# Kernel optimization log

Measured on AMD Instinct MI355X. Metric: run time of the kernel, lower is better.

Reference implementation:

```python
import jax, jax.numpy as jnp
import numpy as np

NUM_CHUNKS = 8
IGNORE_INDEX = -100


def setup_inputs() -> dict:
    key = jax.random.key(0)
    k1, k2, k3, k4 = jax.random.split(key, 4)
    B, S, D, V = 4, 1024, 2048, 32000
    outputs = jax.random.normal(k1, (B, S, D), dtype=jnp.float32)
    weight = jax.random.normal(k2, (V, D), dtype=jnp.float32) * 0.02
    targets = jax.random.randint(k3, (B, S), 0, V)
    ign = jax.random.uniform(k4, (B, S)) < 0.1
    targets = jnp.where(ign, IGNORE_INDEX, targets)
    return {"outputs": outputs, "targets": targets, "weight": weight}


def reference(outputs, targets, weight):
    # outputs: [B, S, D]  targets: [B, S]  weight: [V, D]
    B, S, D = outputs.shape
    x = outputs.reshape(-1, D)          # [N, D]
    t = targets.reshape(-1)             # [N]
    N = x.shape[0]
    n = N // NUM_CHUNKS
    xc = x.reshape(NUM_CHUNKS, n, D)
    tc = t.reshape(NUM_CHUNKS, n)

    def chunk_step(carry, inp):
        xi, ti = inp                       # [n, D], [n]
        valid = ti != IGNORE_INDEX
        ts = jnp.where(valid, ti, 0)
        logits = jnp.einsum('nd,vd->nv', xi, weight)   # [n, V] per-chunk only
        lse = jax.nn.logsumexp(logits, axis=-1)        # [n]
        tgt = jnp.take_along_axis(logits, ts[:, None], axis=-1)[:, 0]
        loss = jnp.where(valid, lse - tgt, 0.0)
        s, cnt = carry
        return (s + loss.sum(), cnt + valid.sum()), None

    init = (jnp.float32(0.0), jnp.int32(0))
    (total, cnt), _ = jax.lax.scan(chunk_step, init, (xc, tc))
    # 'mean' reduction over non-ignored tokens
    return total / jnp.maximum(cnt, 1).astype(total.dtype)
```

## Files before the change

### kernel.cpp

```cpp
#include <hip/hip_runtime.h>
#include <hip/hip_bf16.h>
#include <math.h>

#define IGNORE_INDEX (-100)

typedef unsigned short u16;
typedef unsigned char u8;
typedef int i32x4 __attribute__((ext_vector_type(4)));
typedef int i32x8 __attribute__((ext_vector_type(8)));
typedef float f32x16 __attribute__((ext_vector_type(16)));

#define B_  4
#define S_  1024
#define D_  2048
#define V_  32000
#define N_  (B_ * S_)
#define BM  128
#define BN  128
#define BK  64
#define NTK (D_ / BK)
#define NBM (N_ / BM)
#define NBV (V_ / BN)
#define NWG (NBM * NBV)
#define BUFB 16384
#define XSC 16.0f
#define WSC 64.0f
#define DSC (1.0f / (XSC * WSC))

static __device__ __forceinline__ u8 f2e4m3(float f) {
  unsigned u = __float_as_uint(f);
  unsigned s = (u >> 24) & 0x80;
  float a = fabsf(f);
  if (a > 448.f) return (u8)(s | 0x7E);
  if (a < 0.015625f) {
    int d = __float2int_rn(a * 512.f);
    return (u8)(s | (unsigned)d);
  }
  unsigned au = u & 0x7FFFFFFF;
  au += 0x7FFFF + ((au >> 20) & 1);
  int e = (int)(au >> 23) - 127;
  if (e > 8) return (u8)(s | 0x7E);
  unsigned code = (unsigned)((e + 7) << 3) | ((au >> 20) & 7);
  if (code >= 0x7F) code = 0x7E;
  return (u8)(s | code);
}

static __device__ __forceinline__ int swz(int b) { return b ^ (((b >> 7) & 7) << 4); }

__device__ __forceinline__ void gload_lds16(const u8* g, char* l) {
  __builtin_amdgcn_global_load_lds(
      (const __attribute__((address_space(1))) unsigned int*)g,
      (__attribute__((address_space(3))) unsigned int*)l, 16, 0, 0);
}

__global__ void cast_fp8_kernel(const float* __restrict__ x, const float* __restrict__ w,
                                uint4* __restrict__ xb, uint4* __restrict__ wb) {
  const int GX = N_ * (D_ / 16);
  const int GW = V_ * (D_ / 16);
  int gi = blockIdx.x * blockDim.x + threadIdx.x;
  int stride = gridDim.x * blockDim.x;
  for (; gi < GX + GW; gi += stride) {
    const float* src;
    uint4* dst;
    float sc;
    int g0;
    if (gi < GX) { src = x; dst = xb; sc = XSC; g0 = gi; }
    else         { src = w; dst = wb; sc = WSC; g0 = gi - GX; }
    const float4* p = (const float4*)(src + (size_t)g0 * 16);
    float4 v0 = p[0], v1 = p[1], v2 = p[2], v3 = p[3];
    unsigned w0 = (unsigned)f2e4m3(v0.x * sc) | ((unsigned)f2e4m3(v0.y * sc) << 8) |
                  ((unsigned)f2e4m3(v0.z * sc) << 16) | ((unsigned)f2e4m3(v0.w * sc) << 24);
    unsigned w1 = (unsigned)f2e4m3(v1.x * sc) | ((unsigned)f2e4m3(v1.y * sc) << 8) |
                  ((unsigned)f2e4m3(v1.z * sc) << 16) | ((unsigned)f2e4m3(v1.w * sc) << 24);
    unsigned w2 = (unsigned)f2e4m3(v2.x * sc) | ((unsigned)f2e4m3(v2.y * sc) << 8) |
                  ((unsigned)f2e4m3(v2.z * sc) << 16) | ((unsigned)f2e4m3(v2.w * sc) << 24);
    unsigned w3 = (unsigned)f2e4m3(v3.x * sc) | ((unsigned)f2e4m3(v3.y * sc) << 8) |
                  ((unsigned)f2e4m3(v3.z * sc) << 16) | ((unsigned)f2e4m3(v3.w * sc) << 24);
    dst[g0] = make_uint4(w0, w1, w2, w3);
  }
}

__global__ void tgt_kernel(const float* __restrict__ x, const int* __restrict__ tg,
                           const float* __restrict__ w, float* __restrict__ tgt_out) {
  int wid = threadIdx.x >> 6;
  int lane = threadIdx.x & 63;
  int row = blockIdx.x * 4 + wid;
  int t = tg[row];
  int tt = (t == IGNORE_INDEX) ? 0 : t;
  const float4* xr = (const float4*)(x + (size_t)row * D_);
  const float4* wr = (const float4*)(w + (size_t)tt * D_);
  float s = 0.f;
#pragma unroll
  for (int i = 0; i < D_ / 4 / 64; ++i) {
    float4 a = xr[lane + i * 64];
    float4 b = wr[lane + i * 64];
    s += a.x * b.x + a.y * b.y + a.z * b.z + a.w * b.w;
  }
#pragma unroll
  for (int off = 32; off > 0; off >>= 1) s += __shfl_xor(s, off);
  if (lane == 0) tgt_out[row] = (t == IGNORE_INDEX) ? 0.f : s;
}

__launch_bounds__(256, 4)
__global__ void gemm_lse_kernel(const u8* __restrict__ Xb, const u8* __restrict__ Wb,
                                float* __restrict__ partials) {
  __shared__ __align__(16) char lds[2 * BUFB + 256 * sizeof(float)];
  float* redf = (float*)(lds + 2 * BUFB);

  int phys = blockIdx.x;
  int orig = (phys & 7) * (NWG / 8) + (phys >> 3);
  int mb = orig & (NBM - 1);
  int nb = orig >> 5;
  int m0 = mb * BM, n0 = nb * BN;
  int t = threadIdx.x, lane = t & 63;
  int wid = t >> 6, wm = wid >> 1, wn = wid & 1;

  const u8* srcR[4];
  {
#pragma unroll
    for (int r = 0; r < 4; ++r) {
      int b = r * 4096 + t * 16;
      int l = swz(b);
      if (r < 2) srcR[r] = Xb + (size_t)(m0 + (l >> 6)) * D_ + (l & 63);
      else       srcR[r] = Wb + (size_t)(n0 + ((l - 8192) >> 6)) * D_ + (l & 63);
    }
  }
  int dstw = wid * 1024;

#define STAGE(buf, kb)                                                        \
  do {                                                                        \
    _Pragma("unroll") for (int r_ = 0; r_ < 4; ++r_)                          \
        gload_lds16(srcR[r_] + (kb),                                          \
                    (char*)lds + (buf) * BUFB + r_ * 4096 + dstw);            \
  } while (0)

  int offA[2][2], offB[2][2];
#pragma unroll
  for (int f = 0; f < 2; ++f) {
    int b = (wm * 64 + f * 32 + (lane & 31)) * 64 + (lane >> 5) * 32;
    offA[f][0] = swz(b);
    offA[f][1] = swz(b + 16);
  }
#pragma unroll
  for (int n = 0; n < 2; ++n) {
    int b = 8192 + (wn * 64 + n * 32 + (lane & 31)) * 64 + (lane >> 5) * 32;
    offB[n][0] = swz(b);
    offB[n][1] = swz(b + 16);
  }

#define RD32(dst, base, o)                                           \
  do {                                                               \
    i32x4 lo_ = *(const i32x4*)((base) + (o)[0]);                    \
    i32x4 hi_ = *(const i32x4*)((base) + (o)[1]);                    \
    dst = __builtin_shufflevector(lo_, hi_, 0, 1, 2, 3, 4, 5, 6, 7); \
  } while (0)

  f32x16 acc[2][2];
#pragma unroll
  for (int m = 0; m < 2; ++m)
#pragma unroll
    for (int n = 0; n < 2; ++n)
      acc[m][n] = (f32x16){0.f, 0.f, 0.f, 0.f, 0.f, 0.f, 0.f, 0.f,
                           0.f, 0.f, 0.f, 0.f, 0.f, 0.f, 0.f, 0.f};

  const int sc1 = 0x7F7F7F7F;

  STAGE(0, 0);
  STAGE(1, BK);

  for (int tt = 0; tt < NTK; ++tt) {
    const char* rbase = (const char*)lds + (tt & 1) * BUFB;
    if (tt < NTK - 1) asm volatile("s_waitcnt vmcnt(4)" ::: "memory");
    else              asm volatile("s_waitcnt vmcnt(0)" ::: "memory");
    __builtin_amdgcn_s_barrier();
    __builtin_amdgcn_sched_barrier(0);
    i32x8 af[2], bf[2];
    RD32(af[0], rbase, offA[0]);
    RD32(af[1], rbase, offA[1]);
    RD32(bf[0], rbase, offB[0]);
    RD32(bf[1], rbase, offB[1]);
    asm volatile("s_waitcnt lgkmcnt(0)" ::: "memory");
    __builtin_amdgcn_sched_barrier(0);
    __builtin_amdgcn_s_barrier();
    __builtin_amdgcn_sched_barrier(0);
    if (tt < NTK - 2) STAGE(tt & 1, (tt + 2) * BK);
    __builtin_amdgcn_s_setprio(1);
    acc[0][0] = __builtin_amdgcn_mfma_scale_f32_32x32x64_f8f6f4(
        af[0], bf[0], acc[0][0], 0, 0, 0, sc1, 0, sc1);
    acc[0][1] = __builtin_amdgcn_mfma_scale_f32_32x32x64_f8f6f4(
        af[0], bf[1], acc[0][1], 0, 0, 0, sc1, 0, sc1);
    acc[1][0] = __builtin_amdgcn_mfma_scale_f32_32x32x64_f8f6f4(
        af[1], bf[0], acc[1][0], 0, 0, 0, sc1, 0, sc1);
    acc[1][1] = __builtin_amdgcn_mfma_scale_f32_32x32x64_f8f6f4(
        af[1], bf[1], acc[1][1], 0, 0, 0, sc1, 0, sc1);
    __builtin_amdgcn_s_setprio(0);
  }

#pragma unroll
  for (int m = 0; m < 2; ++m) {
#pragma unroll
    for (int r = 0; r < 16; ++r) {
      float e = __expf(acc[m][0][r] * DSC) + __expf(acc[m][1][r] * DSC);
#pragma unroll
      for (int off = 1; off < 32; off <<= 1) e += __shfl_xor(e, off);
      if ((lane & 31) == 0) {
        int row32 = (r & 3) + 8 * (r >> 2) + 4 * (lane >> 5);
        redf[wn * 128 + wm * 64 + m * 32 + row32] = e;
      }
    }
  }
  __syncthreads();
  if (t < BM) {
    partials[(size_t)nb * N_ + (m0 + t)] = redf[t] + redf[128 + t];
  }
#undef STAGE
#undef RD32
}

__global__ void reduce_kernel(const float* __restrict__ partials, const float* __restrict__ tgt,
                              const int* __restrict__ tg, float2* __restrict__ bsum) {
  int row = blockIdx.x * blockDim.x + threadIdx.x;
  float S = 0.f;
  for (int nb = 0; nb < NBV; ++nb) S += partials[(size_t)nb * N_ + row];
  float lse = logf(S);
  bool valid = tg[row] != IGNORE_INDEX;
  float loss = valid ? (lse - tgt[row]) : 0.f;
  float cnt = valid ? 1.f : 0.f;
#pragma unroll
  for (int off = 32; off > 0; off >>= 1) {
    loss += __shfl_xor(loss, off);
    cnt += __shfl_xor(cnt, off);
  }
  __shared__ float ls[4], cs[4];
  int lane = threadIdx.x & 63, w = threadIdx.x >> 6;
  if (lane == 0) { ls[w] = loss; cs[w] = cnt; }
  __syncthreads();
  if (threadIdx.x == 0)
    bsum[blockIdx.x] = make_float2(ls[0] + ls[1] + ls[2] + ls[3], cs[0] + cs[1] + cs[2] + cs[3]);
}

__global__ void finalize_kernel(const float2* __restrict__ bsum, float* __restrict__ out) {
  float s = 0.f, c = 0.f;
  for (int i = 0; i < N_ / 256; ++i) { s += bsum[i].x; c += bsum[i].y; }
  out[0] = s / fmaxf(c, 1.f);
}

extern "C" void kernel_launch(void* const* d_in, const int* in_sizes, int n_in,
                              void* d_out, int out_size, void* d_ws, size_t ws_size,
                              hipStream_t stream) {
  const float* x = (const float*)d_in[0];
  const int* tg = (const int*)d_in[1];
  const float* w = (const float*)d_in[2];
  float* out = (float*)d_out;

  char* ws = (char*)d_ws;
  u8* Xb = (u8*)ws;
  u8* Wb = (u8*)(ws + (size_t)N_ * D_);
  float* partials = (float*)(ws + (size_t)N_ * D_ + (size_t)V_ * D_);
  float* tgt = (float*)((char*)partials + (size_t)NBV * N_ * sizeof(float));
  float2* bsum = (float2*)(tgt + N_);

  cast_fp8_kernel<<<4096, 256, 0, stream>>>(x, w, (uint4*)Xb, (uint4*)Wb);
  tgt_kernel<<<N_ / 4, 256, 0, stream>>>(x, tg, w, tgt);
  gemm_lse_kernel<<<NWG, 256, 0, stream>>>(Xb, Wb, partials);
  reduce_kernel<<<N_ / 256, 256, 0, stream>>>(partials, tgt, tg, bsum);
  finalize_kernel<<<1, 1, 0, stream>>>(bsum, out);
}
```

Baseline: 424.6 us.

## Triple-buffer LDS and prefetch MFMA fragments one k-step ahead

Moves the GEMM main loop from two to three LDS stages and unrolls it by two with ping-pong register fragments. Each iteration now reads the next tile's fragments from LDS while the MFMAs for the current tile run, and it drops one of the two barriers per k-step. The aim is to hide LDS read latency and global-load latency behind matrix-core work. In exchange it uses more LDS and registers, and the occupancy hint drops from 4 to 3 workgroups per CU.

```diff
diff --git a/kernel.cpp b/kernel.cpp
--- a/kernel.cpp
+++ b/kernel.cpp
@@ -101,11 +101,11 @@
   if (lane == 0) tgt_out[row] = (t == IGNORE_INDEX) ? 0.f : s;
 }
 
-__launch_bounds__(256, 4)
+__launch_bounds__(256, 3)
 __global__ void gemm_lse_kernel(const u8* __restrict__ Xb, const u8* __restrict__ Wb,
                                 float* __restrict__ partials) {
-  __shared__ __align__(16) char lds[2 * BUFB + 256 * sizeof(float)];
-  float* redf = (float*)(lds + 2 * BUFB);
+  __shared__ __align__(16) char lds[3 * BUFB + 256 * sizeof(float)];
+  float* redf = (float*)(lds + 3 * BUFB);
 
   int phys = blockIdx.x;
   int orig = (phys & 7) * (NWG / 8) + (phys >> 3);
@@ -154,6 +154,25 @@
     i32x4 hi_ = *(const i32x4*)((base) + (o)[1]);                    \
     dst = __builtin_shufflevector(lo_, hi_, 0, 1, 2, 3, 4, 5, 6, 7); \
   } while (0)
+#define READF(AF, BF, rbuf)                               \
+  do {                                                    \
+    const char* rb_ = (const char*)lds + (rbuf) * BUFB;   \
+    RD32(AF[0], rb_, offA[0]);                            \
+    RD32(AF[1], rb_, offA[1]);                            \
+    RD32(BF[0], rb_, offB[0]);                            \
+    RD32(BF[1], rb_, offB[1]);                            \
+  } while (0)
+#define MFMA4(AF, BF)                                                \
+  do {                                                               \
+    acc[0][0] = __builtin_amdgcn_mfma_scale_f32_32x32x64_f8f6f4(     \
+        AF[0], BF[0], acc[0][0], 0, 0, 0, sc1, 0, sc1);              \
+    acc[0][1] = __builtin_amdgcn_mfma_scale_f32_32x32x64_f8f6f4(     \
+        AF[0], BF[1], acc[0][1], 0, 0, 0, sc1, 0, sc1);              \
+    acc[1][0] = __builtin_amdgcn_mfma_scale_f32_32x32x64_f8f6f4(     \
+        AF[1], BF[0], acc[1][0], 0, 0, 0, sc1, 0, sc1);              \
+    acc[1][1] = __builtin_amdgcn_mfma_scale_f32_32x32x64_f8f6f4(     \
+        AF[1], BF[1], acc[1][1], 0, 0, 0, sc1, 0, sc1);              \
+  } while (0)
 
   f32x16 acc[2][2];
 #pragma unroll
@@ -165,35 +184,49 @@
 
   const int sc1 = 0x7F7F7F7F;
 
+  i32x8 aE[2], bE[2], aO[2], bO[2];
+
   STAGE(0, 0);
   STAGE(1, BK);
-
-  for (int tt = 0; tt < NTK; ++tt) {
-    const char* rbase = (const char*)lds + (tt & 1) * BUFB;
-    if (tt < NTK - 1) asm volatile("s_waitcnt vmcnt(4)" ::: "memory");
-    else              asm volatile("s_waitcnt vmcnt(0)" ::: "memory");
-    __builtin_amdgcn_s_barrier();
-    __builtin_amdgcn_sched_barrier(0);
-    i32x8 af[2], bf[2];
-    RD32(af[0], rbase, offA[0]);
-    RD32(af[1], rbase, offA[1]);
-    RD32(bf[0], rbase, offB[0]);
-    RD32(bf[1], rbase, offB[1]);
-    asm volatile("s_waitcnt lgkmcnt(0)" ::: "memory");
-    __builtin_amdgcn_sched_barrier(0);
-    __builtin_amdgcn_s_barrier();
-    __builtin_amdgcn_sched_barrier(0);
-    if (tt < NTK - 2) STAGE(tt & 1, (tt + 2) * BK);
-    __builtin_amdgcn_s_setprio(1);
-    acc[0][0] = __builtin_amdgcn_mfma_scale_f32_32x32x64_f8f6f4(
-        af[0], bf[0], acc[0][0], 0, 0, 0, sc1, 0, sc1);
-    acc[0][1] = __builtin_amdgcn_mfma_scale_f32_32x32x64_f8f6f4(
-        af[0], bf[1], acc[0][1], 0, 0, 0, sc1, 0, sc1);
-    acc[1][0] = __builtin_amdgcn_mfma_scale_f32_32x32x64_f8f6f4(
-        af[1], bf[0], acc[1][0], 0, 0, 0, sc1, 0, sc1);
-    acc[1][1] = __builtin_amdgcn_mfma_scale_f32_32x32x64_f8f6f4(
-        af[1], bf[1], acc[1][1], 0, 0, 0, sc1, 0, sc1);
-    __builtin_amdgcn_s_setprio(0);
+  STAGE(2, 2 * BK);
+  asm volatile("s_waitcnt vmcnt(8)" ::: "memory");
+  __builtin_amdgcn_s_barrier();
+  __builtin_amdgcn_sched_barrier(0);
+  READF(aE, bE, 0);
+
+  int b = 0;
+  for (int i = 0; i < 16; ++i) {
+    {
+      const int tt = 2 * i;
+      asm volatile("s_waitcnt lgkmcnt(0)" ::: "memory");
+      if (i < 15) asm volatile("s_waitcnt vmcnt(4)" ::: "memory");
+      else        asm volatile("s_waitcnt vmcnt(0)" ::: "memory");
+      __builtin_amdgcn_s_barrier();
+      __builtin_amdgcn_sched_barrier(0);
+      const int rb = (b == 2) ? 0 : b + 1;
+      if (tt < 29) STAGE(b, (tt + 3) * BK);
+      READF(aO, bO, rb);
+      __builtin_amdgcn_sched_barrier(0);
+      __builtin_amdgcn_s_setprio(1);
+      MFMA4(aE, bE);
+      __builtin_amdgcn_s_setprio(0);
+      b = rb;
+    }
+    {
+      const int tt = 2 * i + 1;
+      asm volatile("s_waitcnt lgkmcnt(0)" ::: "memory");
+      if (tt <= 29) asm volatile("s_waitcnt vmcnt(4)" ::: "memory");
+      __builtin_amdgcn_s_barrier();
+      __builtin_amdgcn_sched_barrier(0);
+      const int rb = (b == 2) ? 0 : b + 1;
+      if (tt < 29) STAGE(b, (tt + 3) * BK);
+      if (tt < 31) READF(aE, bE, rb);
+      __builtin_amdgcn_sched_barrier(0);
+      __builtin_amdgcn_s_setprio(1);
+      MFMA4(aO, bO);
+      __builtin_amdgcn_s_setprio(0);
+      b = rb;
+    }
   }
 
 #pragma unroll
@@ -215,6 +248,8 @@
   }
 #undef STAGE
 #undef RD32
+#undef READF
+#undef MFMA4
 }
 
 __global__ void reduce_kernel(const float* __restrict__ partials, const float* __restrict__ tgt,
```

New measurement: 1.260 ms. 2.97x slower.

## Pre-swizzle FP8 operands into MFMA fragment layout and load directly to registers

Applied to the files above, without the earlier changes.

The cast kernel now writes X and W in a fragment-major layout that matches the MFMA 32x32x64 register operand order. The GEMM drops the LDS double-buffer staging, barriers and swizzled LDS reads, and instead loads each wave's fragments straight from global memory into registers with a one-step software prefetch. This removes LDS traffic and synchronisation but gives up reuse of tiles across waves through LDS, so each wave fetches its operands from global/L2 independently. Launch bounds occupancy hint is lowered to 1.

```diff
diff --git a/kernel.cpp b/kernel.cpp
--- a/kernel.cpp
+++ b/kernel.cpp
@@ -17,12 +17,10 @@
 #define N_  (B_ * S_)
 #define BM  128
 #define BN  128
-#define BK  64
-#define NTK (D_ / BK)
+#define NTK 32
 #define NBM (N_ / BM)
 #define NBV (V_ / BN)
 #define NWG (NBM * NBV)
-#define BUFB 16384
 #define XSC 16.0f
 #define WSC 64.0f
 #define DSC (1.0f / (XSC * WSC))
@@ -45,16 +43,13 @@
   return (u8)(s | code);
 }
 
-static __device__ __forceinline__ int swz(int b) { return b ^ (((b >> 7) & 7) << 4); }
-
-__device__ __forceinline__ void gload_lds16(const u8* g, char* l) {
-  __builtin_amdgcn_global_load_lds(
-      (const __attribute__((address_space(1))) unsigned int*)g,
-      (__attribute__((address_space(3))) unsigned int*)l, 16, 0, 0);
+static __device__ __forceinline__ unsigned pack4(float4 v, float sc) {
+  return (unsigned)f2e4m3(v.x * sc) | ((unsigned)f2e4m3(v.y * sc) << 8) |
+         ((unsigned)f2e4m3(v.z * sc) << 16) | ((unsigned)f2e4m3(v.w * sc) << 24);
 }
 
 __global__ void cast_fp8_kernel(const float* __restrict__ x, const float* __restrict__ w,
-                                uint4* __restrict__ xb, uint4* __restrict__ wb) {
+                                uint4* __restrict__ xf, uint4* __restrict__ wf) {
   const int GX = N_ * (D_ / 16);
   const int GW = V_ * (D_ / 16);
   int gi = blockIdx.x * blockDim.x + threadIdx.x;
@@ -64,19 +59,17 @@
     uint4* dst;
     float sc;
     int g0;
-    if (gi < GX) { src = x; dst = xb; sc = XSC; g0 = gi; }
-    else         { src = w; dst = wb; sc = WSC; g0 = gi - GX; }
-    const float4* p = (const float4*)(src + (size_t)g0 * 16);
+    if (gi < GX) { src = x; dst = xf; sc = XSC; g0 = gi; }
+    else         { src = w; dst = wf; sc = WSC; g0 = gi - GX; }
+    int R = g0 >> 7, idx = g0 & 127;
+    int c = idx * 16;
+    int kt = c >> 6, kc = c & 63;
+    int lane = ((kc >> 5) << 5) | (R & 31);
+    int fb = R >> 5;
+    const float4* p = (const float4*)(src + (size_t)R * D_ + c);
     float4 v0 = p[0], v1 = p[1], v2 = p[2], v3 = p[3];
-    unsigned w0 = (unsigned)f2e4m3(v0.x * sc) | ((unsigned)f2e4m3(v0.y * sc) << 8) |
-                  ((unsigned)f2e4m3(v0.z * sc) << 16) | ((unsigned)f2e4m3(v0.w * sc) << 24);
-    unsigned w1 = (unsigned)f2e4m3(v1.x * sc) | ((unsigned)f2e4m3(v1.y * sc) << 8) |
-                  ((unsigned)f2e4m3(v1.z * sc) << 16) | ((unsigned)f2e4m3(v1.w * sc) << 24);
-    unsigned w2 = (unsigned)f2e4m3(v2.x * sc) | ((unsigned)f2e4m3(v2.y * sc) << 8) |
-                  ((unsigned)f2e4m3(v2.z * sc) << 16) | ((unsigned)f2e4m3(v2.w * sc) << 24);
-    unsigned w3 = (unsigned)f2e4m3(v3.x * sc) | ((unsigned)f2e4m3(v3.y * sc) << 8) |
-                  ((unsigned)f2e4m3(v3.z * sc) << 16) | ((unsigned)f2e4m3(v3.w * sc) << 24);
-    dst[g0] = make_uint4(w0, w1, w2, w3);
+    uint4 o = make_uint4(pack4(v0, sc), pack4(v1, sc), pack4(v2, sc), pack4(v3, sc));
+    dst[((size_t)fb * 32 + kt) * 128 + lane * 2 + ((kc >> 4) & 1)] = o;
   }
 }
 
@@ -101,59 +94,25 @@
   if (lane == 0) tgt_out[row] = (t == IGNORE_INDEX) ? 0.f : s;
 }
 
-__launch_bounds__(256, 4)
-__global__ void gemm_lse_kernel(const u8* __restrict__ Xb, const u8* __restrict__ Wb,
+__launch_bounds__(256, 1)
+__global__ void gemm_lse_kernel(const uint4* __restrict__ Xf, const uint4* __restrict__ Wf,
                                 float* __restrict__ partials) {
-  __shared__ __align__(16) char lds[2 * BUFB + 256 * sizeof(float)];
-  float* redf = (float*)(lds + 2 * BUFB);
+  __shared__ float redf[256];
 
   int phys = blockIdx.x;
   int orig = (phys & 7) * (NWG / 8) + (phys >> 3);
   int mb = orig & (NBM - 1);
   int nb = orig >> 5;
-  int m0 = mb * BM, n0 = nb * BN;
+  int m0 = mb * BM;
   int t = threadIdx.x, lane = t & 63;
   int wid = t >> 6, wm = wid >> 1, wn = wid & 1;
 
-  const u8* srcR[4];
-  {
-#pragma unroll
-    for (int r = 0; r < 4; ++r) {
-      int b = r * 4096 + t * 16;
-      int l = swz(b);
-      if (r < 2) srcR[r] = Xb + (size_t)(m0 + (l >> 6)) * D_ + (l & 63);
-      else       srcR[r] = Wb + (size_t)(n0 + ((l - 8192) >> 6)) * D_ + (l & 63);
-    }
-  }
-  int dstw = wid * 1024;
-
-#define STAGE(buf, kb)                                                        \
-  do {                                                                        \
-    _Pragma("unroll") for (int r_ = 0; r_ < 4; ++r_)                          \
-        gload_lds16(srcR[r_] + (kb),                                          \
-                    (char*)lds + (buf) * BUFB + r_ * 4096 + dstw);            \
-  } while (0)
-
-  int offA[2][2], offB[2][2];
-#pragma unroll
-  for (int f = 0; f < 2; ++f) {
-    int b = (wm * 64 + f * 32 + (lane & 31)) * 64 + (lane >> 5) * 32;
-    offA[f][0] = swz(b);
-    offA[f][1] = swz(b + 16);
-  }
-#pragma unroll
-  for (int n = 0; n < 2; ++n) {
-    int b = 8192 + (wn * 64 + n * 32 + (lane & 31)) * 64 + (lane >> 5) * 32;
-    offB[n][0] = swz(b);
-    offB[n][1] = swz(b + 16);
-  }
-
-#define RD32(dst, base, o)                                           \
-  do {                                                               \
-    i32x4 lo_ = *(const i32x4*)((base) + (o)[0]);                    \
-    i32x4 hi_ = *(const i32x4*)((base) + (o)[1]);                    \
-    dst = __builtin_shufflevector(lo_, hi_, 0, 1, 2, 3, 4, 5, 6, 7); \
-  } while (0)
+  int afb = mb * 4 + wm * 2;
+  int bfb = nb * 4 + wn * 2;
+  const i32x8* A0 = (const i32x8*)(Xf + (size_t)afb * 32 * 128) + lane;
+  const i32x8* A1 = A0 + 32 * 64;
+  const i32x8* B0 = (const i32x8*)(Wf + (size_t)bfb * 32 * 128) + lane;
+  const i32x8* B1 = B0 + 32 * 64;
 
   f32x16 acc[2][2];
 #pragma unroll
@@ -165,35 +124,25 @@
 
   const int sc1 = 0x7F7F7F7F;
 
-  STAGE(0, 0);
-  STAGE(1, BK);
-
-  for (int tt = 0; tt < NTK; ++tt) {
-    const char* rbase = (const char*)lds + (tt & 1) * BUFB;
-    if (tt < NTK - 1) asm volatile("s_waitcnt vmcnt(4)" ::: "memory");
-    else              asm volatile("s_waitcnt vmcnt(0)" ::: "memory");
-    __builtin_amdgcn_s_barrier();
-    __builtin_amdgcn_sched_barrier(0);
-    i32x8 af[2], bf[2];
-    RD32(af[0], rbase, offA[0]);
-    RD32(af[1], rbase, offA[1]);
-    RD32(bf[0], rbase, offB[0]);
-    RD32(bf[1], rbase, offB[1]);
-    asm volatile("s_waitcnt lgkmcnt(0)" ::: "memory");
-    __builtin_amdgcn_sched_barrier(0);
-    __builtin_amdgcn_s_barrier();
-    __builtin_amdgcn_sched_barrier(0);
-    if (tt < NTK - 2) STAGE(tt & 1, (tt + 2) * BK);
+  i32x8 a0 = A0[0], a1 = A1[0], b0 = B0[0], b1 = B1[0];
+#pragma unroll 4
+  for (int kt = 0; kt < NTK; ++kt) {
+    i32x8 na0, na1, nb0, nb1;
+    if (kt < NTK - 1) {
+      int e = (kt + 1) * 64;
+      na0 = A0[e]; na1 = A1[e]; nb0 = B0[e]; nb1 = B1[e];
+    }
     __builtin_amdgcn_s_setprio(1);
     acc[0][0] = __builtin_amdgcn_mfma_scale_f32_32x32x64_f8f6f4(
-        af[0], bf[0], acc[0][0], 0, 0, 0, sc1, 0, sc1);
+        a0, b0, acc[0][0], 0, 0, 0, sc1, 0, sc1);
     acc[0][1] = __builtin_amdgcn_mfma_scale_f32_32x32x64_f8f6f4(
-        af[0], bf[1], acc[0][1], 0, 0, 0, sc1, 0, sc1);
+        a0, b1, acc[0][1], 0, 0, 0, sc1, 0, sc1);
     acc[1][0] = __builtin_amdgcn_mfma_scale_f32_32x32x64_f8f6f4(
-        af[1], bf[0], acc[1][0], 0, 0, 0, sc1, 0, sc1);
+        a1, b0, acc[1][0], 0, 0, 0, sc1, 0, sc1);
     acc[1][1] = __builtin_amdgcn_mfma_scale_f32_32x32x64_f8f6f4(
-        af[1], bf[1], acc[1][1], 0, 0, 0, sc1, 0, sc1);
+        a1, b1, acc[1][1], 0, 0, 0, sc1, 0, sc1);
     __builtin_amdgcn_s_setprio(0);
+    a0 = na0; a1 = na1; b0 = nb0; b1 = nb1;
   }
 
 #pragma unroll
@@ -213,8 +162,6 @@
   if (t < BM) {
     partials[(size_t)nb * N_ + (m0 + t)] = redf[t] + redf[128 + t];
   }
-#undef STAGE
-#undef RD32
 }
 
 __global__ void reduce_kernel(const float* __restrict__ partials, const float* __restrict__ tgt,
@@ -254,15 +201,15 @@
   float* out = (float*)d_out;
 
   char* ws = (char*)d_ws;
-  u8* Xb = (u8*)ws;
-  u8* Wb = (u8*)(ws + (size_t)N_ * D_);
+  uint4* Xf = (uint4*)ws;
+  uint4* Wf = (uint4*)(ws + (size_t)N_ * D_);
   float* partials = (float*)(ws + (size_t)N_ * D_ + (size_t)V_ * D_);
   float* tgt = (float*)((char*)partials + (size_t)NBV * N_ * sizeof(float));
   float2* bsum = (float2*)(tgt + N_);
 
-  cast_fp8_kernel<<<4096, 256, 0, stream>>>(x, w, (uint4*)Xb, (uint4*)Wb);
+  cast_fp8_kernel<<<4096, 256, 0, stream>>>(x, w, Xf, Wf);
   tgt_kernel<<<N_ / 4, 256, 0, stream>>>(x, tg, w, tgt);
-  gemm_lse_kernel<<<NWG, 256, 0, stream>>>(Xb, Wb, partials);
+  gemm_lse_kernel<<<NWG, 256, 0, stream>>>(Xf, Wf, partials);
   reduce_kernel<<<N_ / 256, 256, 0, stream>>>(partials, tgt, tg, bsum);
   finalize_kernel<<<1, 1, 0, stream>>>(bsum, out);
 }
```

Measured after the change: 439.2 us. 3.4% more time.
